# Kernel tuning notes

Hardware: AMD Instinct MI355X
Metric: run time of the kernel (lower is better)

The kernel has to match this reference:

```python
import jax, jax.numpy as jnp
import numpy as np

B, SQ, SKV, D, H = 4, 2048, 2048, 1024, 16
DH = D // H  # 64


def setup_inputs() -> dict:
    key = jax.random.key(0)
    ks = jax.random.split(key, 8)
    s = 0.02  # realistic init scale for weights
    return {
        "query": jax.random.normal(ks[0], (B, SQ, D), dtype=jnp.float32),
        "value": jax.random.normal(ks[1], (B, SKV, D), dtype=jnp.float32),
        "wq": jax.random.normal(ks[2], (H, D, DH), dtype=jnp.float32) * s,
        "bq": jnp.zeros((H, DH), dtype=jnp.float32),
        "wk": jax.random.normal(ks[3], (H, D, DH), dtype=jnp.float32) * s,
        "bk": jnp.zeros((H, DH), dtype=jnp.float32),
        "wv": jax.random.normal(ks[4], (H, D, DH), dtype=jnp.float32) * s,
        "bv": jnp.zeros((H, DH), dtype=jnp.float32),
        "wo": jax.random.normal(ks[5], (D, D), dtype=jnp.float32) * s,
        "bo": jnp.zeros((D,), dtype=jnp.float32),
    }


def reference(query, value, wq, bq, wk, bk, wv, bv, wo, bo):
    # Batched equivalent of the per-head Dense loop: [B,S,D] x [H,D,DH] -> [B,H,S,DH]
    q = jnp.einsum("bsd,hde->bhse", query, wq) + bq[None, :, None, :]
    k = jnp.einsum("bsd,hde->bhse", value, wk) + bk[None, :, None, :]
    v = jnp.einsum("bsd,hde->bhse", value, wv) + bv[None, :, None, :]
    scale = 1.0 / jnp.sqrt(jnp.asarray(DH, dtype=q.dtype))
    scores = jnp.einsum("bhqe,bhke->bhqk", q, k) * scale  # [B,H,SQ,SKV]
    align = jax.nn.softmax(scores, axis=-1)
    heads = jnp.einsum("bhqk,bhke->bhqe", align, v)  # [B,H,SQ,DH]
    # concat heads along feature dim (head order preserved)
    heads = jnp.transpose(heads, (0, 2, 1, 3)).reshape(B, SQ, D)
    return heads @ wo + bo
```

## Files before the change

kernel.cpp:

```cpp
#include <hip/hip_runtime.h>
#include <stdint.h>

#define DEVI __device__ __forceinline__

typedef __bf16  bf16x8 __attribute__((ext_vector_type(8)));
typedef float   f32x4  __attribute__((ext_vector_type(4)));
typedef float   f32x16 __attribute__((ext_vector_type(16)));
typedef uint32_t u32x4 __attribute__((ext_vector_type(4)));
typedef uint32_t u32x2v __attribute__((ext_vector_type(2)));
typedef uint16_t u16x8 __attribute__((ext_vector_type(8)));
typedef uint16_t u16x4 __attribute__((ext_vector_type(4)));

static constexpr int BB = 4, SQL = 2048, SKVL = 2048, DMODEL = 1024, NH = 16;
static constexpr int MROWS = BB * SQL;
static constexpr int KD = DMODEL;

DEVI uint16_t f2bf(float x) {
  uint32_t u = __builtin_bit_cast(uint32_t, x);
  u += 0x7FFFu + ((u >> 16) & 1u);
  return (uint16_t)(u >> 16);
}
DEVI uint32_t cvt2bf(float a, float b) {
  __bf16 x = (__bf16)a, y = (__bf16)b;
  return (uint32_t)__builtin_bit_cast(uint16_t, x) |
         ((uint32_t)__builtin_bit_cast(uint16_t, y) << 16);
}
DEVI f32x4 mfma16(bf16x8 a, bf16x8 b, f32x4 c) {
  return __builtin_amdgcn_mfma_f32_16x16x32_bf16(a, b, c, 0, 0, 0);
}
DEVI f32x16 mfma32(bf16x8 a, bf16x8 b, f32x16 c) {
  return __builtin_amdgcn_mfma_f32_32x32x16_bf16(a, b, c, 0, 0, 0);
}
DEVI void gload16(const void* g, void* l) {
  __builtin_amdgcn_global_load_lds((__attribute__((address_space(1))) const void*)g,
                                   (__attribute__((address_space(3))) void*)l, 16, 0, 0);
}
DEVI bf16x8 ldread(const void* p) { return __builtin_bit_cast(bf16x8, *(const u32x4*)p); }
DEVI u32x2v plswap(uint32_t a, uint32_t b) {
  return __builtin_amdgcn_permlane32_swap(a, b, false, false);
}

__global__ __launch_bounds__(256) void k_cvt_act(const float* __restrict__ q, const float* __restrict__ v,
                                                 uint16_t* __restrict__ aq, uint16_t* __restrict__ av) {
  const int64_t n4 = (int64_t)MROWS * DMODEL / 4;
  for (int64_t i = (int64_t)blockIdx.x * 256 + threadIdx.x; i < 2 * n4; i += (int64_t)gridDim.x * 256) {
    const bool second = (i >= n4);
    const int64_t j = second ? i - n4 : i;
    const float4 x = (second ? (const float4*)v : (const float4*)q)[j];
    u16x4 o = { f2bf(x.x), f2bf(x.y), f2bf(x.z), f2bf(x.w) };
    *(u16x4*)((second ? av : aq) + j * 4) = o;
  }
}

__global__ __launch_bounds__(256) void k_cvt_w(const float* __restrict__ wq, const float* __restrict__ wk,
                                               const float* __restrict__ wv, const float* __restrict__ wo,
                                               uint16_t* __restrict__ wt) {
  const int idx = blockIdx.x * 256 + threadIdx.x;
  const int z = idx >> 20, f = idx & 1048575;
  const int n = f >> 10, d = f & 1023;
  const float* w = (z == 0) ? wq : (z == 1) ? wk : (z == 2) ? wv : wo;
  const float x = (z < 3) ? w[((n >> 6) << 16) + d * 64 + (n & 63)] : w[d * 1024 + n];
  wt[(size_t)z * 1048576 + f] = f2bf(x);
}

template <int MODE>
__global__ __launch_bounds__(256) void k_gemm(const uint16_t* __restrict__ A, const uint16_t* __restrict__ Bt,
                                              const float* __restrict__ bias, const float* __restrict__ biasB,
                                              void* __restrict__ outp, void* __restrict__ outpB,
                                              float oscale) {
  __shared__ __align__(16) uint16_t Al[128 * 64];
  __shared__ __align__(16) uint16_t Bl[128 * 64];
  const int tid = threadIdx.x;
  const int w = tid >> 6, ln = tid & 63;
  const int g = ln >> 4, lc = ln & 15;
  const int m0 = blockIdx.x * 128, n0 = blockIdx.y * 128;
  const int wm = (w >> 1) * 64, wn = (w & 1) * 64;
  const int srow = w * 32 + (ln >> 3);
  const int colp = (ln & 7) * 16;

  f32x4 acc[4][4] = {};

  for (int kt = 0; kt < KD / 64; ++kt) {
    #pragma unroll
    for (int i = 0; i < 4; ++i) {
      const int row = srow + i * 8;
      const int colb = colp ^ ((row & 7) << 4);
      gload16((const char*)(A + (size_t)(m0 + row) * KD + kt * 64) + colb,
              (char*)Al + w * 4096 + i * 1024);
      gload16((const char*)(Bt + (size_t)(n0 + row) * KD + kt * 64) + colb,
              (char*)Bl + w * 4096 + i * 1024);
    }
    __syncthreads();
    #pragma unroll
    for (int kk = 0; kk < 2; ++kk) {
      bf16x8 af[4], bfr[4];
      #pragma unroll
      for (int mt = 0; mt < 4; ++mt) {
        const int row = wm + mt * 16 + lc;
        af[mt] = ldread((const char*)Al + row * 128 + ((kk * 64 + g * 16) ^ ((row & 7) << 4)));
      }
      #pragma unroll
      for (int nt = 0; nt < 4; ++nt) {
        const int row = wn + nt * 16 + lc;
        bfr[nt] = ldread((const char*)Bl + row * 128 + ((kk * 64 + g * 16) ^ ((row & 7) << 4)));
      }
      #pragma unroll
      for (int mt = 0; mt < 4; ++mt)
        #pragma unroll
        for (int nt = 0; nt < 4; ++nt)
          acc[mt][nt] = mfma16(af[mt], bfr[nt], acc[mt][nt]);
    }
    __syncthreads();
  }
  #pragma unroll
  for (int nt = 0; nt < 4; ++nt) {
    const int n = n0 + wn + nt * 16 + lc;
    const int z = (MODE == 2) ? (n >> 10) : 0;
    const int nn = (MODE == 2) ? (n & 1023) : n;
    const float bv = (MODE == 2) ? (z ? biasB : bias)[nn] : bias[n];
    uint16_t* dst16 = (uint16_t*)((MODE == 2 && z) ? outpB : outp);
    #pragma unroll
    for (int mt = 0; mt < 4; ++mt) {
      #pragma unroll
      for (int r = 0; r < 4; ++r) {
        const int m = m0 + wm + mt * 16 + g * 4 + r;
        if (MODE != 1) {
          float val = acc[mt][nt][r] + bv;
          if (MODE == 0) val *= oscale;
          const int b = m >> 11, s = m & 2047, h = nn >> 6, e = nn & 63;
          dst16[((size_t)((b * NH + h) * SQL + s)) * 64 + e] = f2bf(val);
        } else {
          ((float*)outp)[(size_t)m * DMODEL + n] = acc[mt][nt][r] + bv;
        }
      }
    }
  }
}

__global__ __launch_bounds__(512, 4) void k_attn(const uint16_t* __restrict__ Qb,
                                                 const uint16_t* __restrict__ Kb,
                                                 const uint16_t* __restrict__ Vb,
                                                 uint16_t* __restrict__ Hd) {
  __shared__ __align__(16) uint16_t Kl[2][64 * 64];
  __shared__ __align__(16) uint16_t Vl[2][64 * 64];
  const int tid = threadIdx.x;
  const int w = tid >> 6, ln = tid & 63;
  const int ql = ln & 31, hi = ln >> 5;
  const int bh = blockIdx.y;
  const int q0 = blockIdx.x * 256 + w * 32;

  const uint16_t* Qp = Qb + ((size_t)bh * SQL + q0 + ql) * 64;
  bf16x8 qf[4];
  #pragma unroll
  for (int s = 0; s < 4; ++s)
    qf[s] = __builtin_bit_cast(bf16x8, *(const u16x8*)(Qp + s * 16 + hi * 8));

  const uint16_t* Kbase = Kb + (size_t)bh * SKVL * 64;
  const uint16_t* Vbase = Vb + (size_t)bh * SKVL * 64;

  const int swl = (ln & 7) << 4;
  const int e0off = (hi << 4) ^ swl;
  const int rb = ql * 128;

  const bool kstage = (w < 4);
  const int krow0 = (w & 3) * 16 + (ln >> 3);
  const int kcolb = (((ln & 7) ^ (ln >> 3)) << 4);
  const int t2 = tid & 255;
  const int vkv = (t2 & 31) * 2, ve0 = (t2 >> 5) * 8;

  f32x16 acc0 = {}, acc1 = {};
  float lsum = 0.f;

  if (kstage) {
    #pragma unroll
    for (int i = 0; i < 2; ++i) {
      const int row = krow0 + i * 8;
      gload16((const char*)(Kbase + (size_t)row * 64) + kcolb,
              (char*)&Kl[0][0] + (w & 3) * 2048 + i * 1024);
    }
  } else {
    const u16x8 a = *(const u16x8*)(Vbase + (size_t)vkv * 64 + ve0);
    const u16x8 b = *(const u16x8*)(Vbase + (size_t)(vkv + 1) * 64 + ve0);
    #pragma unroll
    for (int i = 0; i < 8; ++i) {
      const int e = ve0 + i;
      *(uint32_t*)((char*)&Vl[0][0] + e * 128 + ((vkv * 2) ^ ((e & 7) << 4))) =
          (uint32_t)a[i] | ((uint32_t)b[i] << 16);
    }
  }
  __syncthreads();

  int cur = 0;
  for (int t = 0; t < SKVL / 64; ++t) {
    const bool pre = (t + 1 < SKVL / 64);
    u16x8 nv0, nv1;
    if (pre) {
      if (kstage) {
        const uint16_t* Kc = Kbase + (size_t)(t + 1) * 4096;
        #pragma unroll
        for (int i = 0; i < 2; ++i) {
          const int row = krow0 + i * 8;
          gload16((const char*)(Kc + (size_t)row * 64) + kcolb,
                  (char*)&Kl[cur ^ 1][0] + (w & 3) * 2048 + i * 1024);
        }
      } else {
        const uint16_t* Vc = Vbase + (size_t)(t + 1) * 4096;
        nv0 = *(const u16x8*)(Vc + (size_t)vkv * 64 + ve0);
        nv1 = *(const u16x8*)(Vc + (size_t)(vkv + 1) * 64 + ve0);
      }
    }
    const char* Kc0 = (const char*)&Kl[cur][0];
    f32x16 s0 = {}, s1 = {};
    __builtin_amdgcn_s_setprio(1);
    #pragma unroll
    for (int s = 0; s < 4; ++s) {
      const int off = e0off ^ (s << 5);
      const bf16x8 k0 = ldread(Kc0 + rb + off);
      const bf16x8 k1 = ldread(Kc0 + 4096 + rb + off);
      s0 = mfma32(k0, qf[s], s0);
      s1 = mfma32(k1, qf[s], s1);
    }
    __builtin_amdgcn_s_setprio(0);
    float ps = 0.f;
    #pragma unroll
    for (int r = 0; r < 16; ++r) {
      s0[r] = __builtin_amdgcn_exp2f(s0[r]);
      s1[r] = __builtin_amdgcn_exp2f(s1[r]);
      ps += s0[r] + s1[r];
    }
    lsum += ps;
    uint32_t w32[2][4][2];
    #pragma unroll
    for (int c8 = 0; c8 < 4; ++c8) {
      #pragma unroll
      for (int p = 0; p < 2; ++p) {
        w32[0][c8][p] = cvt2bf(s0[4 * c8 + 2 * p], s0[4 * c8 + 2 * p + 1]);
        w32[1][c8][p] = cvt2bf(s1[4 * c8 + 2 * p], s1[4 * c8 + 2 * p + 1]);
      }
    }
    const char* Vc0 = (const char*)&Vl[cur][0];
    __builtin_amdgcn_s_setprio(1);
    #pragma unroll
    for (int u = 0; u < 4; ++u) {
      const int tt = u >> 1, ul = u & 1;
      const u32x2v e0 = plswap(w32[tt][2 * ul][0], w32[tt][2 * ul + 1][0]);
      const u32x2v e1 = plswap(w32[tt][2 * ul][1], w32[tt][2 * ul + 1][1]);
      u32x4 pj;
      pj[0] = e0[0]; pj[1] = e1[0]; pj[2] = e0[1]; pj[3] = e1[1];
      const bf16x8 pb = __builtin_bit_cast(bf16x8, pj);
      const int off = e0off ^ (u << 5);
      const bf16x8 v0 = ldread(Vc0 + rb + off);
      const bf16x8 v1 = ldread(Vc0 + 4096 + rb + off);
      acc0 = mfma32(v0, pb, acc0);
      acc1 = mfma32(v1, pb, acc1);
    }
    __builtin_amdgcn_s_setprio(0);
    if (pre && !kstage) {
      #pragma unroll
      for (int i = 0; i < 8; ++i) {
        const int e = ve0 + i;
        *(uint32_t*)((char*)&Vl[cur ^ 1][0] + e * 128 + ((vkv * 2) ^ ((e & 7) << 4))) =
            (uint32_t)nv0[i] | ((uint32_t)nv1[i] << 16);
      }
    }
    __syncthreads();
    cur ^= 1;
  }
  const float lt = lsum + __shfl_xor(lsum, 32);
  const float inv = __builtin_amdgcn_rcpf(lt);
  const int b = bh >> 4, h = bh & 15;
  uint16_t* op = Hd + ((size_t)(b * SQL + q0 + ql)) * DMODEL + h * 64;
  #pragma unroll
  for (int et = 0; et < 2; ++et) {
    #pragma unroll
    for (int r2 = 0; r2 < 8; ++r2) {
      const float v0 = (et ? acc1[2 * r2] : acc0[2 * r2]) * inv;
      const float v1 = (et ? acc1[2 * r2 + 1] : acc0[2 * r2 + 1]) * inv;
      const int e = et * 32 + 4 * hi + (r2 & 1) * 2 + (r2 >> 1) * 8;
      *(uint32_t*)(op + e) = cvt2bf(v0, v1);
    }
  }
}

extern "C" void kernel_launch(void* const* d_in, const int* in_sizes, int n_in,
                              void* d_out, int out_size, void* d_ws, size_t ws_size,
                              hipStream_t stream) {
  const float* query = (const float*)d_in[0];
  const float* value = (const float*)d_in[1];
  const float* wq = (const float*)d_in[2];
  const float* bq = (const float*)d_in[3];
  const float* wk = (const float*)d_in[4];
  const float* bk = (const float*)d_in[5];
  const float* wv = (const float*)d_in[6];
  const float* bv = (const float*)d_in[7];
  const float* wo = (const float*)d_in[8];
  const float* bo = (const float*)d_in[9];

  const size_t SZ_ACT = (size_t)MROWS * DMODEL * 2;
  const size_t SZ_W   = (size_t)4 * DMODEL * DMODEL * 2;
  if (ws_size < 6 * SZ_ACT + SZ_W) return;

  char* ws = (char*)d_ws;
  uint16_t* Aq = (uint16_t*)ws;  ws += SZ_ACT;
  uint16_t* Av = (uint16_t*)ws;  ws += SZ_ACT;
  uint16_t* Wt = (uint16_t*)ws;  ws += SZ_W;
  uint16_t* Qb = (uint16_t*)ws;  ws += SZ_ACT;
  uint16_t* Kb = (uint16_t*)ws;  ws += SZ_ACT;
  uint16_t* Vb = (uint16_t*)ws;  ws += SZ_ACT;
  uint16_t* Hd = (uint16_t*)ws;  ws += SZ_ACT;

  const float QSCALE = 0.18033688011112042f;

  k_cvt_act<<<dim3(2048), dim3(256), 0, stream>>>(query, value, Aq, Av);
  k_cvt_w<<<dim3(16384), dim3(256), 0, stream>>>(wq, wk, wv, wo, Wt);
  k_gemm<0><<<dim3(64, 8), dim3(256), 0, stream>>>(Aq, Wt, bq, nullptr, Qb, nullptr, QSCALE);
  k_gemm<2><<<dim3(64, 16), dim3(256), 0, stream>>>(Av, Wt + 1048576, bk, bv, Kb, Vb, 1.0f);
  k_attn<<<dim3(8, 64), dim3(512), 0, stream>>>(Qb, Kb, Vb, Hd);
  k_gemm<1><<<dim3(64, 8), dim3(256), 0, stream>>>(Hd, Wt + 3145728, bo, nullptr, d_out, nullptr, 1.0f);
}
```

Baseline: 219.8 us.

## Process two query tiles per wave in attention to reuse K/V LDS reads

The attention block shrinks from 8 to 4 waves, and each wave now handles 64 query rows as two 32-row tiles. Every K and V fragment read from LDS feeds both tiles, which halves LDS read traffic per MFMA. All threads now stage both K and V, where before the waves were split into K-loaders and V-loaders. The cost is roughly double the accumulator and score registers per wave and fewer waves per block to hide latency.

```diff
diff --git a/kernel.cpp b/kernel.cpp
--- a/kernel.cpp
+++ b/kernel.cpp
@@ -137,7 +137,7 @@
   }
 }
 
-__global__ __launch_bounds__(512, 4) void k_attn(const uint16_t* __restrict__ Qb,
+__global__ __launch_bounds__(256, 2) void k_attn(const uint16_t* __restrict__ Qb,
                                                  const uint16_t* __restrict__ Kb,
                                                  const uint16_t* __restrict__ Vb,
                                                  uint16_t* __restrict__ Hd) {
@@ -147,13 +147,16 @@
   const int w = tid >> 6, ln = tid & 63;
   const int ql = ln & 31, hi = ln >> 5;
   const int bh = blockIdx.y;
-  const int q0 = blockIdx.x * 256 + w * 32;
-
-  const uint16_t* Qp = Qb + ((size_t)bh * SQL + q0 + ql) * 64;
-  bf16x8 qf[4];
+  const int q0 = blockIdx.x * 256 + w * 64;
+
+  bf16x8 qf[2][4];
   #pragma unroll
-  for (int s = 0; s < 4; ++s)
-    qf[s] = __builtin_bit_cast(bf16x8, *(const u16x8*)(Qp + s * 16 + hi * 8));
+  for (int qt = 0; qt < 2; ++qt) {
+    const uint16_t* Qp = Qb + ((size_t)bh * SQL + q0 + qt * 32 + ql) * 64;
+    #pragma unroll
+    for (int s = 0; s < 4; ++s)
+      qf[qt][s] = __builtin_bit_cast(bf16x8, *(const u16x8*)(Qp + s * 16 + hi * 8));
+  }
 
   const uint16_t* Kbase = Kb + (size_t)bh * SKVL * 64;
   const uint16_t* Vbase = Vb + (size_t)bh * SKVL * 64;
@@ -162,23 +165,20 @@
   const int e0off = (hi << 4) ^ swl;
   const int rb = ql * 128;
 
-  const bool kstage = (w < 4);
-  const int krow0 = (w & 3) * 16 + (ln >> 3);
+  const int krow0 = w * 16 + (ln >> 3);
   const int kcolb = (((ln & 7) ^ (ln >> 3)) << 4);
-  const int t2 = tid & 255;
-  const int vkv = (t2 & 31) * 2, ve0 = (t2 >> 5) * 8;
-
-  f32x16 acc0 = {}, acc1 = {};
-  float lsum = 0.f;
-
-  if (kstage) {
+  const int vkv = (tid & 31) * 2, ve0 = (tid >> 5) * 8;
+
+  f32x16 acc[2][2] = {};
+  float lsum0 = 0.f, lsum1 = 0.f;
+
+  {
     #pragma unroll
     for (int i = 0; i < 2; ++i) {
       const int row = krow0 + i * 8;
       gload16((const char*)(Kbase + (size_t)row * 64) + kcolb,
-              (char*)&Kl[0][0] + (w & 3) * 2048 + i * 1024);
-    }
-  } else {
+              (char*)&Kl[0][0] + w * 2048 + i * 1024);
+    }
     const u16x8 a = *(const u16x8*)(Vbase + (size_t)vkv * 64 + ve0);
     const u16x8 b = *(const u16x8*)(Vbase + (size_t)(vkv + 1) * 64 + ve0);
     #pragma unroll
@@ -195,47 +195,47 @@
     const bool pre = (t + 1 < SKVL / 64);
     u16x8 nv0, nv1;
     if (pre) {
-      if (kstage) {
-        const uint16_t* Kc = Kbase + (size_t)(t + 1) * 4096;
+      const uint16_t* Kc = Kbase + (size_t)(t + 1) * 4096;
+      #pragma unroll
+      for (int i = 0; i < 2; ++i) {
+        const int row = krow0 + i * 8;
+        gload16((const char*)(Kc + (size_t)row * 64) + kcolb,
+                (char*)&Kl[cur ^ 1][0] + w * 2048 + i * 1024);
+      }
+      const uint16_t* Vc = Vbase + (size_t)(t + 1) * 4096;
+      nv0 = *(const u16x8*)(Vc + (size_t)vkv * 64 + ve0);
+      nv1 = *(const u16x8*)(Vc + (size_t)(vkv + 1) * 64 + ve0);
+    }
+    const char* Kc0 = (const char*)&Kl[cur][0];
+    uint32_t w32[2][2][4][2];
+    #pragma unroll
+    for (int qt = 0; qt < 2; ++qt) {
+      f32x16 s0 = {}, s1 = {};
+      __builtin_amdgcn_s_setprio(1);
+      #pragma unroll
+      for (int s = 0; s < 4; ++s) {
+        const int off = e0off ^ (s << 5);
+        const bf16x8 k0 = ldread(Kc0 + rb + off);
+        const bf16x8 k1 = ldread(Kc0 + 4096 + rb + off);
+        s0 = mfma32(k0, qf[qt][s], s0);
+        s1 = mfma32(k1, qf[qt][s], s1);
+      }
+      __builtin_amdgcn_s_setprio(0);
+      float ps = 0.f;
+      #pragma unroll
+      for (int r = 0; r < 16; ++r) {
+        s0[r] = __builtin_amdgcn_exp2f(s0[r]);
+        s1[r] = __builtin_amdgcn_exp2f(s1[r]);
+        ps += s0[r] + s1[r];
+      }
+      if (qt == 0) lsum0 += ps; else lsum1 += ps;
+      #pragma unroll
+      for (int c8 = 0; c8 < 4; ++c8) {
         #pragma unroll
-        for (int i = 0; i < 2; ++i) {
-          const int row = krow0 + i * 8;
-          gload16((const char*)(Kc + (size_t)row * 64) + kcolb,
-                  (char*)&Kl[cur ^ 1][0] + (w & 3) * 2048 + i * 1024);
+        for (int p = 0; p < 2; ++p) {
+          w32[qt][0][c8][p] = cvt2bf(s0[4 * c8 + 2 * p], s0[4 * c8 + 2 * p + 1]);
+          w32[qt][1][c8][p] = cvt2bf(s1[4 * c8 + 2 * p], s1[4 * c8 + 2 * p + 1]);
         }
-      } else {
-        const uint16_t* Vc = Vbase + (size_t)(t + 1) * 4096;
-        nv0 = *(const u16x8*)(Vc + (size_t)vkv * 64 + ve0);
-        nv1 = *(const u16x8*)(Vc + (size_t)(vkv + 1) * 64 + ve0);
-      }
-    }
-    const char* Kc0 = (const char*)&Kl[cur][0];
-    f32x16 s0 = {}, s1 = {};
-    __builtin_amdgcn_s_setprio(1);
-    #pragma unroll
-    for (int s = 0; s < 4; ++s) {
-      const int off = e0off ^ (s << 5);
-      const bf16x8 k0 = ldread(Kc0 + rb + off);
-      const bf16x8 k1 = ldread(Kc0 + 4096 + rb + off);
-      s0 = mfma32(k0, qf[s], s0);
-      s1 = mfma32(k1, qf[s], s1);
-    }
-    __builtin_amdgcn_s_setprio(0);
-    float ps = 0.f;
-    #pragma unroll
-    for (int r = 0; r < 16; ++r) {
-      s0[r] = __builtin_amdgcn_exp2f(s0[r]);
-      s1[r] = __builtin_amdgcn_exp2f(s1[r]);
-      ps += s0[r] + s1[r];
-    }
-    lsum += ps;
-    uint32_t w32[2][4][2];
-    #pragma unroll
-    for (int c8 = 0; c8 < 4; ++c8) {
-      #pragma unroll
-      for (int p = 0; p < 2; ++p) {
-        w32[0][c8][p] = cvt2bf(s0[4 * c8 + 2 * p], s0[4 * c8 + 2 * p + 1]);
-        w32[1][c8][p] = cvt2bf(s1[4 * c8 + 2 * p], s1[4 * c8 + 2 * p + 1]);
       }
     }
     const char* Vc0 = (const char*)&Vl[cur][0];
@@ -243,19 +243,22 @@
     #pragma unroll
     for (int u = 0; u < 4; ++u) {
       const int tt = u >> 1, ul = u & 1;
-      const u32x2v e0 = plswap(w32[tt][2 * ul][0], w32[tt][2 * ul + 1][0]);
-      const u32x2v e1 = plswap(w32[tt][2 * ul][1], w32[tt][2 * ul + 1][1]);
-      u32x4 pj;
-      pj[0] = e0[0]; pj[1] = e1[0]; pj[2] = e0[1]; pj[3] = e1[1];
-      const bf16x8 pb = __builtin_bit_cast(bf16x8, pj);
       const int off = e0off ^ (u << 5);
       const bf16x8 v0 = ldread(Vc0 + rb + off);
       const bf16x8 v1 = ldread(Vc0 + 4096 + rb + off);
-      acc0 = mfma32(v0, pb, acc0);
-      acc1 = mfma32(v1, pb, acc1);
+      #pragma unroll
+      for (int qt = 0; qt < 2; ++qt) {
+        const u32x2v e0 = plswap(w32[qt][tt][2 * ul][0], w32[qt][tt][2 * ul + 1][0]);
+        const u32x2v e1 = plswap(w32[qt][tt][2 * ul][1], w32[qt][tt][2 * ul + 1][1]);
+        u32x4 pj;
+        pj[0] = e0[0]; pj[1] = e1[0]; pj[2] = e0[1]; pj[3] = e1[1];
+        const bf16x8 pb = __builtin_bit_cast(bf16x8, pj);
+        acc[qt][0] = mfma32(v0, pb, acc[qt][0]);
+        acc[qt][1] = mfma32(v1, pb, acc[qt][1]);
+      }
     }
     __builtin_amdgcn_s_setprio(0);
-    if (pre && !kstage) {
+    if (pre) {
       #pragma unroll
       for (int i = 0; i < 8; ++i) {
         const int e = ve0 + i;
@@ -266,18 +269,22 @@
     __syncthreads();
     cur ^= 1;
   }
-  const float lt = lsum + __shfl_xor(lsum, 32);
-  const float inv = __builtin_amdgcn_rcpf(lt);
   const int b = bh >> 4, h = bh & 15;
-  uint16_t* op = Hd + ((size_t)(b * SQL + q0 + ql)) * DMODEL + h * 64;
   #pragma unroll
-  for (int et = 0; et < 2; ++et) {
-    #pragma unroll
-    for (int r2 = 0; r2 < 8; ++r2) {
-      const float v0 = (et ? acc1[2 * r2] : acc0[2 * r2]) * inv;
-      const float v1 = (et ? acc1[2 * r2 + 1] : acc0[2 * r2 + 1]) * inv;
-      const int e = et * 32 + 4 * hi + (r2 & 1) * 2 + (r2 >> 1) * 8;
-      *(uint32_t*)(op + e) = cvt2bf(v0, v1);
+  for (int qt = 0; qt < 2; ++qt) {
+    const float ls = qt ? lsum1 : lsum0;
+    const float lt = ls + __shfl_xor(ls, 32);
+    const float inv = __builtin_amdgcn_rcpf(lt);
+    uint16_t* op = Hd + ((size_t)(b * SQL + q0 + qt * 32 + ql)) * DMODEL + h * 64;
+    #pragma unroll
+    for (int et = 0; et < 2; ++et) {
+      #pragma unroll
+      for (int r2 = 0; r2 < 8; ++r2) {
+        const float v0 = acc[qt][et][2 * r2] * inv;
+        const float v1 = acc[qt][et][2 * r2 + 1] * inv;
+        const int e = et * 32 + 4 * hi + (r2 & 1) * 2 + (r2 >> 1) * 8;
+        *(uint32_t*)(op + e) = cvt2bf(v0, v1);
+      }
     }
   }
 }
@@ -315,6 +322,6 @@
   k_cvt_w<<<dim3(16384), dim3(256), 0, stream>>>(wq, wk, wv, wo, Wt);
   k_gemm<0><<<dim3(64, 8), dim3(256), 0, stream>>>(Aq, Wt, bq, nullptr, Qb, nullptr, QSCALE);
   k_gemm<2><<<dim3(64, 16), dim3(256), 0, stream>>>(Av, Wt + 1048576, bk, bv, Kb, Vb, 1.0f);
-  k_attn<<<dim3(8, 64), dim3(512), 0, stream>>>(Qb, Kb, Vb, Hd);
+  k_attn<<<dim3(8, 64), dim3(256), 0, stream>>>(Qb, Kb, Vb, Hd);
   k_gemm<1><<<dim3(64, 8), dim3(256), 0, stream>>>(Hd, Wt + 3145728, bo, nullptr, d_out, nullptr, 1.0f);
 }
```

Measured after the change: 220.8 us. Within noise of the previous version (+0.5%).
